# Kernel tuning notes

Hardware: AMD Instinct MI355X
Metric: run time of the kernel (lower is better)

The kernel has to match this reference:

```python
import jax, jax.numpy as jnp
import numpy as np

B, DIN, DH, DOUT = 256, 784, 512, 10


def _softplus(x):
    # matches torch.log(1.0 + torch.exp(x)) exactly
    return jnp.log(1.0 + jnp.exp(x))


def _kl(w_mu, w_sigma_sp, size_in):
    # compute_kl_loss(w_mu, diag_embed(softplus(w_sigma))) without materializing diag
    # w_mu: (in, out), w_sigma_sp: (out, in)
    trace = jnp.sum(w_sigma_sp, axis=1)            # (out,)
    mu_sq = jnp.sum(w_mu * w_mu, axis=0)           # (out,)
    logdet = jnp.sum(jnp.log(w_sigma_sp), axis=1)  # slogdet of diag = sum log diag
    return 0.5 * jnp.sum(trace + mu_sq - size_in - logdet)


def setup_inputs() -> dict:
    key = jax.random.key(0)
    ks = jax.random.split(key, 9)
    inp = {
        "x": jax.random.normal(ks[0], (B, DIN, 1), dtype=jnp.float32),
        "w_mu1": 5e-5 * jax.random.normal(ks[1], (DIN, DH), dtype=jnp.float32),
        "w_sigma1": jax.random.uniform(ks[2], (DH, DIN), minval=-12.0, maxval=-2.0, dtype=jnp.float32),
        "b_mu1": 5e-5 * jax.random.normal(ks[3], (DH, 1), dtype=jnp.float32),
        "b_sigma1": jax.random.uniform(ks[4], (DH,), minval=-12.0, maxval=-2.0, dtype=jnp.float32),
        "w_mu2": 5e-5 * jax.random.normal(ks[5], (DH, DOUT), dtype=jnp.float32),
        "w_sigma2": jax.random.uniform(ks[6], (DOUT, DH), minval=-12.0, maxval=-2.0, dtype=jnp.float32),
        "b_mu2": 5e-5 * jax.random.normal(ks[7], (DOUT, 1), dtype=jnp.float32),
        "b_sigma2": jax.random.uniform(ks[8], (DOUT,), minval=-12.0, maxval=-2.0, dtype=jnp.float32),
    }
    return inp


def reference(x, w_mu1, w_sigma1, b_mu1, b_sigma1, w_mu2, w_sigma2, b_mu2, b_sigma2):
    batch = x.shape[0]
    eye_h = jnp.eye(DH, dtype=x.dtype)
    eye_o = jnp.eye(DOUT, dtype=x.dtype)

    # ---- RVLinearlayer 1 (sigma_in = None) ----
    xv = x[..., 0]                                   # (B, DIN)
    mu1 = jnp.einsum('io,bi->bo', w_mu1, xv)[:, :, None] + b_mu1   # (B, DH, 1)
    Ws1 = _softplus(w_sigma1)                        # (DH, DIN)
    quad1 = jnp.einsum('hi,bi->bh', Ws1, xv * xv)    # mu_in^T diag(Ws) mu_in per unit
    sigma1 = quad1[:, :, None] * eye_h + jnp.diag(_softplus(b_sigma1))  # (B, DH, DH)
    kl1 = _kl(w_mu1, Ws1, DIN)

    # ---- RVNonLinearFunc (ReLU) ----
    mu2 = jax.nn.relu(mu1)                           # (B, DH, 1)
    g = (mu1[..., 0] > 0).astype(x.dtype)            # Heaviside grad of relu
    sigma2 = sigma1 * (g[:, :, None] * g[:, None, :])

    # ---- RVLinearlayer 2 (with sigma_in) ----
    m2v = mu2[..., 0]                                # (B, DH)
    mu3 = jnp.einsum('ho,bh->bo', w_mu2, m2v)[:, :, None] + b_mu2   # (B, DOUT, 1)
    Ws2 = _softplus(w_sigma2)                        # (DOUT, DH)
    quad2 = jnp.einsum('oh,bh->bo', Ws2, m2v * m2v)  # (B, DOUT)
    # faithful replication of W_Sigma.view(out,-1) @ sigma_in.view(-1,B) then .view(B,out)
    Sflat = sigma2.reshape(DH * DH, batch)           # same row-major view as torch
    diag_rows = Sflat[jnp.arange(DH) * (DH + 1)]     # rows of the diag positions, (DH, B)
    tr = (Ws2 @ diag_rows).reshape(batch, DOUT)      # (out,B) -> row-major (B,out)
    mid = jnp.einsum('ho,bhk,kp->bop', w_mu2, sigma2, w_mu2)  # w_mu2^T Sigma w_mu2
    sigma3 = (tr[:, :, None] * eye_o + mid + quad2[:, :, None] * eye_o
              + jnp.diag(_softplus(b_sigma2)))       # (B, DOUT, DOUT)
    kl2 = _kl(w_mu2, Ws2, DH)

    # ---- RVSoftmax ----
    p = jax.nn.softmax(mu3[..., 0], axis=1)          # (B, DOUT)
    jac = p[:, :, None] * eye_o - p[:, :, None] * p[:, None, :]  # diag(p) - p p^T
    Sigma_out = jnp.einsum('bij,bjk,blk->bil', jac, sigma3, jac)

    return p, Sigma_out, kl1 + kl2
```

## Files before the change

kernel.cpp:

```cpp
#include <hip/hip_runtime.h>
#include <math.h>

#define BATCH 256
#define DIN 784
#define DH 512
#define DOUT 10
#define SPLITS 8
#define KSPL 98

__device__ __forceinline__ float softplus(float x) { return log1pf(expf(x)); }

__global__ __launch_bounds__(256) void prep_kernel(
    const float* __restrict__ w_mu1, const float* __restrict__ w_sigma1,
    const float* __restrict__ w_mu2, const float* __restrict__ w_sigma2,
    float* __restrict__ Ws1T, float* __restrict__ Ws2,
    float* __restrict__ kl_out) {
  __shared__ float tile[32][33];
  __shared__ float rlds[4];
  const int bid = blockIdx.x;
  const int t = threadIdx.x;
  float acc = 0.0f;

  if (bid < 400) {
    const int th = (bid & 15) * 32;
    const int ti = (bid >> 4) * 32;
    const int tx = t & 31, ty = t >> 5;
#pragma unroll
    for (int r = 0; r < 4; r++) {
      const int h = th + ty + r * 8;
      const int i = ti + tx;
      if (i < DIN) {
        const float s = softplus(w_sigma1[h * DIN + i]);
        tile[ty + r * 8][tx] = s;
        acc += s - logf(s);
      }
    }
    __syncthreads();
#pragma unroll
    for (int r = 0; r < 4; r++) {
      const int i = ti + ty + r * 8;
      const int h = th + tx;
      if (i < DIN) Ws1T[i * DH + h] = tile[tx][ty + r * 8];
    }
  } else if (bid < 464) {
    for (int idx = (bid - 400) * 256 + t; idx < DIN * DH; idx += 64 * 256) {
      const float w = w_mu1[idx];
      acc += w * w;
    }
  } else if (bid == 464) {
    for (int idx = t; idx < DOUT * DH; idx += 256) {
      const float s = softplus(w_sigma2[idx]);
      Ws2[idx] = s;
      acc += s - logf(s);
    }
  } else {
    for (int idx = t; idx < DH * DOUT; idx += 256) {
      const float w = w_mu2[idx];
      acc += w * w;
    }
    if (t == 0) acc += -(float)(DIN * DH + DH * DOUT);
  }

  for (int off = 32; off > 0; off >>= 1) acc += __shfl_down(acc, off);
  const int lane = t & 63, wv = t >> 6;
  if (lane == 0) rlds[wv] = acc;
  __syncthreads();
  if (t == 0) {
    atomicAdd(kl_out, 0.5f * (rlds[0] + rlds[1] + rlds[2] + rlds[3]));
  }
}

__global__ __launch_bounds__(256) void gemm1_kernel(
    const float* __restrict__ x, const float* __restrict__ w_mu1,
    const float* __restrict__ Ws1T, float* __restrict__ mu_part,
    float* __restrict__ q_part) {
  __shared__ float xs[16][KSPL];
  const int t = threadIdx.x;
  const int h0 = blockIdx.x * 64;
  const int b0 = blockIdx.y * 16;
  const int s = blockIdx.z;
  const int i0 = s * KSPL;
  const int hl = (t & 31) * 2;
  const int bl = t >> 5;

  float mu00 = 0.f, mu10 = 0.f, mu01 = 0.f, mu11 = 0.f;
  float q00 = 0.f, q10 = 0.f, q01 = 0.f, q11 = 0.f;

  for (int f = t; f < 16 * KSPL; f += 256) {
    const int bb = f / KSPL, kk = f - bb * KSPL;
    xs[bb][kk] = x[(b0 + bb) * DIN + i0 + kk];
  }
  __syncthreads();

  const float2* wm = (const float2*)&w_mu1[(size_t)i0 * DH + h0 + hl];
  const float2* wsp = (const float2*)&Ws1T[(size_t)i0 * DH + h0 + hl];
#pragma unroll 14
  for (int kk = 0; kk < KSPL; kk++) {
    const float2 wmv = wm[kk * (DH / 2)];
    const float2 wsv = wsp[kk * (DH / 2)];
    const float xa = xs[bl][kk];
    const float xb = xs[bl + 8][kk];
    const float xa2 = xa * xa;
    const float xb2 = xb * xb;
    mu00 = fmaf(wmv.x, xa, mu00);
    mu10 = fmaf(wmv.y, xa, mu10);
    mu01 = fmaf(wmv.x, xb, mu01);
    mu11 = fmaf(wmv.y, xb, mu11);
    q00 = fmaf(wsv.x, xa2, q00);
    q10 = fmaf(wsv.y, xa2, q10);
    q01 = fmaf(wsv.x, xb2, q01);
    q11 = fmaf(wsv.y, xb2, q11);
  }

  const int h = h0 + hl;
  const int bA = b0 + bl, bB = b0 + bl + 8;
  const size_t base = (size_t)s * (BATCH * DH);
  float2* mpA = (float2*)&mu_part[base + (size_t)bA * DH + h];
  float2* mpB = (float2*)&mu_part[base + (size_t)bB * DH + h];
  float2* qpA = (float2*)&q_part[base + (size_t)bA * DH + h];
  float2* qpB = (float2*)&q_part[base + (size_t)bB * DH + h];
  *mpA = make_float2(mu00, mu10);
  *mpB = make_float2(mu01, mu11);
  *qpA = make_float2(q00, q10);
  *qpB = make_float2(q01, q11);
}

__global__ __launch_bounds__(256) void layer2_kernel(
    const float* __restrict__ mu_part, const float* __restrict__ q_part,
    const float* __restrict__ b_mu1, const float* __restrict__ b_sigma1,
    const float* __restrict__ w_mu2, const float* __restrict__ Ws2,
    const float* __restrict__ b_mu2, const float* __restrict__ b_sigma2,
    float* __restrict__ out_p, float* __restrict__ out_sigma) {
  const int b = blockIdx.x, t = threadIdx.x;
  __shared__ float red[4][75];
  __shared__ float fin[75];
  __shared__ float mu3[10], pvec[10], trv[10], spb2[10];
  __shared__ float sig[10][10], Tm[10][10], cs[10], rs[10];

  float musum0 = 0.f, musum1 = 0.f, qsum0 = 0.f, qsum1 = 0.f;
#pragma unroll
  for (int s2 = 0; s2 < SPLITS; s2++) {
    const size_t base = (size_t)s2 * (BATCH * DH) + (size_t)b * DH;
    musum0 += mu_part[base + t];
    musum1 += mu_part[base + t + 256];
    qsum0 += q_part[base + t];
    qsum1 += q_part[base + t + 256];
  }

  float m2v[2], d2v[2];
  {
    const float ma0 = musum0 + b_mu1[t];
    const float ma1 = musum1 + b_mu1[t + 256];
    m2v[0] = ma0 > 0.f ? ma0 : 0.f;
    m2v[1] = ma1 > 0.f ? ma1 : 0.f;
    d2v[0] = ma0 > 0.f ? (qsum0 + softplus(b_sigma1[t])) : 0.f;
    d2v[1] = ma1 > 0.f ? (qsum1 + softplus(b_sigma1[t + 256])) : 0.f;
  }

  float acc[75];
#pragma unroll
  for (int i = 0; i < 75; i++) acc[i] = 0.f;

#pragma unroll
  for (int hh = 0; hh < 2; hh++) {
    const int h = t + hh * 256;
    const float m2h = m2v[hh], d2h = d2v[hh];
    const float msq = m2h * m2h;
    float wrow[10];
#pragma unroll
    for (int o = 0; o < 10; o++) wrow[o] = w_mu2[h * 10 + o];
#pragma unroll
    for (int o = 0; o < 10; o++) {
      acc[o] = fmaf(wrow[o], m2h, acc[o]);
      acc[10 + o] = fmaf(Ws2[o * DH + h], msq, acc[10 + o]);
    }
    int idx = 20;
#pragma unroll
    for (int o = 0; o < 10; o++) {
      const float wd = wrow[o] * d2h;
#pragma unroll
      for (int p = o; p < 10; p++) {
        acc[idx] = fmaf(wd, wrow[p], acc[idx]);
        idx++;
      }
    }
  }

  const int lane = t & 63, wv = t >> 6;
#pragma unroll
  for (int j = 0; j < 75; j++) {
    float v = acc[j];
    for (int off = 32; off > 0; off >>= 1) v += __shfl_down(v, off);
    if (lane == 0) red[wv][j] = v;
  }
  __syncthreads();
  if (t < 75) fin[t] = red[0][t] + red[1][t] + red[2][t] + red[3][t];
  __syncthreads();

  if (t < 10) {
    mu3[t] = fin[t] + b_mu2[t];
    spb2[t] = softplus(b_sigma2[t]);
    const int c0 = b * 10 + t;
    const int o2 = c0 >> 8, cc = c0 & 255;
    float mua = b_mu1[cc], qa = 0.f;
    float mub = b_mu1[256 + cc], qb = 0.f;
#pragma unroll
    for (int s2 = 0; s2 < SPLITS; s2++) {
      const size_t base = (size_t)s2 * (BATCH * DH) + (size_t)cc * DH;
      mua += mu_part[base + cc];
      qa += q_part[base + cc];
      mub += mu_part[base + 256 + cc];
      qb += q_part[base + 256 + cc];
    }
    const float d2aa = mua > 0.f ? (qa + softplus(b_sigma1[cc])) : 0.f;
    const float d2bb = mub > 0.f ? (qb + softplus(b_sigma1[256 + cc])) : 0.f;
    trv[t] = Ws2[o2 * DH + 2 * cc] * d2aa + Ws2[o2 * DH + 2 * cc + 1] * d2bb;
  }
  __syncthreads();

  if (t == 0) {
    float mx = mu3[0];
#pragma unroll
    for (int o = 1; o < 10; o++) mx = fmaxf(mx, mu3[o]);
    float e[10], se = 0.f;
#pragma unroll
    for (int o = 0; o < 10; o++) {
      e[o] = expf(mu3[o] - mx);
      se += e[o];
    }
    const float inv = 1.f / se;
#pragma unroll
    for (int o = 0; o < 10; o++) pvec[o] = e[o] * inv;
  }
  __syncthreads();

  if (t < 100) {
    const int o = t / 10, p = t % 10;
    const int i0 = o < p ? o : p, j0 = o < p ? p : o;
    const int idx = 10 * i0 - (i0 * (i0 - 1)) / 2 + (j0 - i0);
    float v = fin[20 + idx];
    if (o == p) v += trv[o] + fin[10 + o] + spb2[o];
    sig[o][p] = v;
  }
  __syncthreads();

  if (t < 10) {
    float s = 0.f;
#pragma unroll
    for (int j = 0; j < 10; j++) s = fmaf(pvec[j], sig[j][t], s);
    cs[t] = s;
  }
  __syncthreads();

  if (t < 100) {
    const int o = t / 10, p = t % 10;
    Tm[o][p] = pvec[o] * (sig[o][p] - cs[p]);
  }
  __syncthreads();

  if (t < 10) {
    float s = 0.f;
#pragma unroll
    for (int k = 0; k < 10; k++) s = fmaf(Tm[t][k], pvec[k], s);
    rs[t] = s;
  }
  __syncthreads();

  if (t < 100) {
    const int o = t / 10, p = t % 10;
    out_sigma[b * 100 + t] = pvec[p] * (Tm[o][p] - rs[o]);
  }
  if (t < 10) out_p[b * 10 + t] = pvec[t];
}

extern "C" void kernel_launch(void* const* d_in, const int* in_sizes, int n_in,
                              void* d_out, int out_size, void* d_ws,
                              size_t ws_size, hipStream_t stream) {
  const float* x = (const float*)d_in[0];
  const float* w_mu1 = (const float*)d_in[1];
  const float* w_sigma1 = (const float*)d_in[2];
  const float* b_mu1 = (const float*)d_in[3];
  const float* b_sigma1 = (const float*)d_in[4];
  const float* w_mu2 = (const float*)d_in[5];
  const float* w_sigma2 = (const float*)d_in[6];
  const float* b_mu2 = (const float*)d_in[7];
  const float* b_sigma2 = (const float*)d_in[8];

  float* out = (float*)d_out;
  float* out_p = out;
  float* out_sigma = out + 2560;
  float* out_kl = out + 28160;

  char* ws = (char*)d_ws;
  float* Ws1T = (float*)ws;
  float* Ws2 = (float*)(ws + (size_t)401408 * 4);
  float* mu_part = (float*)(ws + (size_t)(401408 + 5120) * 4);
  float* q_part =
      (float*)(ws + (size_t)(401408 + 5120 + SPLITS * BATCH * DH) * 4);

  hipMemsetAsync(out_kl, 0, sizeof(float), stream);
  prep_kernel<<<466, 256, 0, stream>>>(w_mu1, w_sigma1, w_mu2, w_sigma2, Ws1T,
                                       Ws2, out_kl);
  gemm1_kernel<<<dim3(8, 16, 8), 256, 0, stream>>>(x, w_mu1, Ws1T, mu_part,
                                                   q_part);
  layer2_kernel<<<256, 256, 0, stream>>>(mu_part, q_part, b_mu1, b_sigma1,
                                         w_mu2, Ws2, b_mu2, b_sigma2, out_p,
                                         out_sigma);
}
```

Measured before the change: 142.6 us.

## Fuse weight-prep softplus and KL reduction into GEMM and layer2 kernels

Removes the separate prep kernel and memset. Each GEMM block now computes softplus of its w_sigma1 tile directly into shared memory, transposed, and designated blocks produce per-block KL partials. Layer2 recomputes softplus of w_sigma2 on the fly and reduces the KL partials deterministically. This saves a launch and the global round trip of Ws1T, but the softplus of w_sigma1 is now recomputed 16 times, once per batch tile, and the w_sigma1 reads are strided.

```diff
diff --git a/kernel.cpp b/kernel.cpp
--- a/kernel.cpp
+++ b/kernel.cpp
@@ -10,71 +10,14 @@
 
 __device__ __forceinline__ float softplus(float x) { return log1pf(expf(x)); }
 
-__global__ __launch_bounds__(256) void prep_kernel(
-    const float* __restrict__ w_mu1, const float* __restrict__ w_sigma1,
-    const float* __restrict__ w_mu2, const float* __restrict__ w_sigma2,
-    float* __restrict__ Ws1T, float* __restrict__ Ws2,
-    float* __restrict__ kl_out) {
-  __shared__ float tile[32][33];
-  __shared__ float rlds[4];
-  const int bid = blockIdx.x;
-  const int t = threadIdx.x;
-  float acc = 0.0f;
-
-  if (bid < 400) {
-    const int th = (bid & 15) * 32;
-    const int ti = (bid >> 4) * 32;
-    const int tx = t & 31, ty = t >> 5;
-#pragma unroll
-    for (int r = 0; r < 4; r++) {
-      const int h = th + ty + r * 8;
-      const int i = ti + tx;
-      if (i < DIN) {
-        const float s = softplus(w_sigma1[h * DIN + i]);
-        tile[ty + r * 8][tx] = s;
-        acc += s - logf(s);
-      }
-    }
-    __syncthreads();
-#pragma unroll
-    for (int r = 0; r < 4; r++) {
-      const int i = ti + ty + r * 8;
-      const int h = th + tx;
-      if (i < DIN) Ws1T[i * DH + h] = tile[tx][ty + r * 8];
-    }
-  } else if (bid < 464) {
-    for (int idx = (bid - 400) * 256 + t; idx < DIN * DH; idx += 64 * 256) {
-      const float w = w_mu1[idx];
-      acc += w * w;
-    }
-  } else if (bid == 464) {
-    for (int idx = t; idx < DOUT * DH; idx += 256) {
-      const float s = softplus(w_sigma2[idx]);
-      Ws2[idx] = s;
-      acc += s - logf(s);
-    }
-  } else {
-    for (int idx = t; idx < DH * DOUT; idx += 256) {
-      const float w = w_mu2[idx];
-      acc += w * w;
-    }
-    if (t == 0) acc += -(float)(DIN * DH + DH * DOUT);
-  }
-
-  for (int off = 32; off > 0; off >>= 1) acc += __shfl_down(acc, off);
-  const int lane = t & 63, wv = t >> 6;
-  if (lane == 0) rlds[wv] = acc;
-  __syncthreads();
-  if (t == 0) {
-    atomicAdd(kl_out, 0.5f * (rlds[0] + rlds[1] + rlds[2] + rlds[3]));
-  }
-}
-
 __global__ __launch_bounds__(256) void gemm1_kernel(
     const float* __restrict__ x, const float* __restrict__ w_mu1,
-    const float* __restrict__ Ws1T, float* __restrict__ mu_part,
-    float* __restrict__ q_part) {
+    const float* __restrict__ w_sigma1, const float* __restrict__ w_mu2,
+    const float* __restrict__ w_sigma2, float* __restrict__ mu_part,
+    float* __restrict__ q_part, float* __restrict__ kl_part) {
   __shared__ float xs[16][KSPL];
+  __shared__ float wst[KSPL][66];
+  __shared__ float rlds[4];
   const int t = threadIdx.x;
   const int h0 = blockIdx.x * 64;
   const int b0 = blockIdx.y * 16;
@@ -83,21 +26,24 @@
   const int hl = (t & 31) * 2;
   const int bl = t >> 5;
 
-  float mu00 = 0.f, mu10 = 0.f, mu01 = 0.f, mu11 = 0.f;
-  float q00 = 0.f, q10 = 0.f, q01 = 0.f, q11 = 0.f;
-
   for (int f = t; f < 16 * KSPL; f += 256) {
     const int bb = f / KSPL, kk = f - bb * KSPL;
     xs[bb][kk] = x[(b0 + bb) * DIN + i0 + kk];
   }
-  __syncthreads();
+  for (int f = t; f < 64 * KSPL; f += 256) {
+    const int hh = f / KSPL, kk = f - hh * KSPL;
+    wst[kk][hh] = softplus(w_sigma1[(h0 + hh) * DIN + i0 + kk]);
+  }
+  __syncthreads();
+
+  float mu00 = 0.f, mu10 = 0.f, mu01 = 0.f, mu11 = 0.f;
+  float q00 = 0.f, q10 = 0.f, q01 = 0.f, q11 = 0.f;
 
   const float2* wm = (const float2*)&w_mu1[(size_t)i0 * DH + h0 + hl];
-  const float2* wsp = (const float2*)&Ws1T[(size_t)i0 * DH + h0 + hl];
 #pragma unroll 14
   for (int kk = 0; kk < KSPL; kk++) {
     const float2 wmv = wm[kk * (DH / 2)];
-    const float2 wsv = wsp[kk * (DH / 2)];
+    const float2 wsv = *(const float2*)&wst[kk][hl];
     const float xa = xs[bl][kk];
     const float xb = xs[bl + 8][kk];
     const float xa2 = xa * xa;
@@ -115,27 +61,59 @@
   const int h = h0 + hl;
   const int bA = b0 + bl, bB = b0 + bl + 8;
   const size_t base = (size_t)s * (BATCH * DH);
-  float2* mpA = (float2*)&mu_part[base + (size_t)bA * DH + h];
-  float2* mpB = (float2*)&mu_part[base + (size_t)bB * DH + h];
-  float2* qpA = (float2*)&q_part[base + (size_t)bA * DH + h];
-  float2* qpB = (float2*)&q_part[base + (size_t)bB * DH + h];
-  *mpA = make_float2(mu00, mu10);
-  *mpB = make_float2(mu01, mu11);
-  *qpA = make_float2(q00, q10);
-  *qpB = make_float2(q01, q11);
+  *(float2*)&mu_part[base + (size_t)bA * DH + h] = make_float2(mu00, mu10);
+  *(float2*)&mu_part[base + (size_t)bB * DH + h] = make_float2(mu01, mu11);
+  *(float2*)&q_part[base + (size_t)bA * DH + h] = make_float2(q00, q10);
+  *(float2*)&q_part[base + (size_t)bB * DH + h] = make_float2(q01, q11);
+
+  float kl = 0.f;
+  int slot = -1;
+  if (blockIdx.y == 0) {
+    for (int f = t; f < 64 * KSPL; f += 256) {
+      const int hh = f / KSPL, kk = f - hh * KSPL;
+      const float sv = wst[kk][hh];
+      kl += sv - logf(sv);
+    }
+    slot = blockIdx.x * 8 + s;
+  } else if (blockIdx.y == 1) {
+#pragma unroll 14
+    for (int kk = 0; kk < KSPL; kk++) {
+      const float2 wmv = wm[kk * (DH / 2)];
+      kl = fmaf(wmv.x, wmv.x, kl);
+      kl = fmaf(wmv.y, wmv.y, kl);
+    }
+    slot = 64 + blockIdx.x * 8 + s;
+  } else if (blockIdx.y == 2 && blockIdx.x == 0) {
+    for (int idx = s * 640 + t; idx < s * 640 + 640; idx += 256) {
+      const float sv = softplus(w_sigma2[idx]);
+      const float wv = w_mu2[idx];
+      kl += sv - logf(sv);
+      kl = fmaf(wv, wv, kl);
+    }
+    slot = 128 + s;
+  }
+
+  for (int off = 32; off > 0; off >>= 1) kl += __shfl_down(kl, off);
+  const int lane = t & 63, wv = t >> 6;
+  if (lane == 0) rlds[wv] = kl;
+  __syncthreads();
+  if (t == 0 && slot >= 0)
+    kl_part[slot] = rlds[0] + rlds[1] + rlds[2] + rlds[3];
 }
 
 __global__ __launch_bounds__(256) void layer2_kernel(
     const float* __restrict__ mu_part, const float* __restrict__ q_part,
     const float* __restrict__ b_mu1, const float* __restrict__ b_sigma1,
-    const float* __restrict__ w_mu2, const float* __restrict__ Ws2,
+    const float* __restrict__ w_mu2, const float* __restrict__ w_sigma2,
     const float* __restrict__ b_mu2, const float* __restrict__ b_sigma2,
-    float* __restrict__ out_p, float* __restrict__ out_sigma) {
+    const float* __restrict__ kl_part, float* __restrict__ out_p,
+    float* __restrict__ out_sigma, float* __restrict__ out_kl) {
   const int b = blockIdx.x, t = threadIdx.x;
   __shared__ float red[4][75];
   __shared__ float fin[75];
   __shared__ float mu3[10], pvec[10], trv[10], spb2[10];
   __shared__ float sig[10][10], Tm[10][10], cs[10], rs[10];
+  __shared__ float klred[4];
 
   float musum0 = 0.f, musum1 = 0.f, qsum0 = 0.f, qsum1 = 0.f;
 #pragma unroll
@@ -172,7 +150,7 @@
 #pragma unroll
     for (int o = 0; o < 10; o++) {
       acc[o] = fmaf(wrow[o], m2h, acc[o]);
-      acc[10 + o] = fmaf(Ws2[o * DH + h], msq, acc[10 + o]);
+      acc[10 + o] = fmaf(softplus(w_sigma2[o * DH + h]), msq, acc[10 + o]);
     }
     int idx = 20;
 #pragma unroll
@@ -214,7 +192,8 @@
     }
     const float d2aa = mua > 0.f ? (qa + softplus(b_sigma1[cc])) : 0.f;
     const float d2bb = mub > 0.f ? (qb + softplus(b_sigma1[256 + cc])) : 0.f;
-    trv[t] = Ws2[o2 * DH + 2 * cc] * d2aa + Ws2[o2 * DH + 2 * cc + 1] * d2bb;
+    trv[t] = softplus(w_sigma2[o2 * DH + 2 * cc]) * d2aa +
+             softplus(w_sigma2[o2 * DH + 2 * cc + 1]) * d2bb;
   }
   __syncthreads();
 
@@ -271,6 +250,15 @@
     out_sigma[b * 100 + t] = pvec[p] * (Tm[o][p] - rs[o]);
   }
   if (t < 10) out_p[b * 10 + t] = pvec[t];
+
+  float klv = (b == 0 && t < 136) ? kl_part[t] : 0.f;
+  for (int off = 32; off > 0; off >>= 1) klv += __shfl_down(klv, off);
+  if (lane == 0) klred[wv] = klv;
+  __syncthreads();
+  if (b == 0 && t == 0) {
+    out_kl[0] =
+        0.5f * (klred[0] + klred[1] + klred[2] + klred[3] - 406528.0f);
+  }
 }
 
 extern "C" void kernel_launch(void* const* d_in, const int* in_sizes, int n_in,
@@ -291,19 +279,14 @@
   float* out_sigma = out + 2560;
   float* out_kl = out + 28160;
 
-  char* ws = (char*)d_ws;
-  float* Ws1T = (float*)ws;
-  float* Ws2 = (float*)(ws + (size_t)401408 * 4);
-  float* mu_part = (float*)(ws + (size_t)(401408 + 5120) * 4);
-  float* q_part =
-      (float*)(ws + (size_t)(401408 + 5120 + SPLITS * BATCH * DH) * 4);
-
-  hipMemsetAsync(out_kl, 0, sizeof(float), stream);
-  prep_kernel<<<466, 256, 0, stream>>>(w_mu1, w_sigma1, w_mu2, w_sigma2, Ws1T,
-                                       Ws2, out_kl);
-  gemm1_kernel<<<dim3(8, 16, 8), 256, 0, stream>>>(x, w_mu1, Ws1T, mu_part,
-                                                   q_part);
+  float* ws = (float*)d_ws;
+  float* mu_part = ws;
+  float* q_part = ws + SPLITS * BATCH * DH;
+  float* kl_part = ws + 2 * SPLITS * BATCH * DH;
+
+  gemm1_kernel<<<dim3(8, 16, 8), 256, 0, stream>>>(
+      x, w_mu1, w_sigma1, w_mu2, w_sigma2, mu_part, q_part, kl_part);
   layer2_kernel<<<256, 256, 0, stream>>>(mu_part, q_part, b_mu1, b_sigma1,
-                                         w_mu2, Ws2, b_mu2, b_sigma2, out_p,
-                                         out_sigma);
+                                         w_mu2, w_sigma2, b_mu2, b_sigma2,
+                                         kl_part, out_p, out_sigma, out_kl);
 }
```

Measured after the change: 141.7 us. Within noise of the previous version (-0.6%).
